# Optimization experiments

Hardware: AMD Instinct MI355X
Metric: run time of the kernel (lower is better)

The kernel has to match this reference:

```python
import jax, jax.numpy as jnp
import numpy as np

D_MODEL = 512
H = 8
D_K = D_MODEL // H
NEG = -1.0e9


def setup_inputs() -> dict:
    key = jax.random.key(0)
    ks = jax.random.split(key, 8)
    B, S = 2, 4096
    q = jax.random.normal(ks[0], (B, S, D_MODEL), dtype=jnp.float32)
    k = jax.random.normal(ks[1], (B, S, D_MODEL), dtype=jnp.float32)
    v = jax.random.normal(ks[2], (B, S, D_MODEL), dtype=jnp.float32)
    mask = jax.random.randint(ks[3], (B, 1, 1, S), 0, 2, dtype=jnp.int32)
    scale = 1.0 / np.sqrt(D_MODEL)
    w_q = jax.random.normal(ks[4], (D_MODEL, D_MODEL), dtype=jnp.float32) * scale
    w_k = jax.random.normal(ks[5], (D_MODEL, D_MODEL), dtype=jnp.float32) * scale
    w_v = jax.random.normal(ks[6], (D_MODEL, D_MODEL), dtype=jnp.float32) * scale
    w_o = jax.random.normal(ks[7], (D_MODEL, D_MODEL), dtype=jnp.float32) * scale
    return {"q": q, "k": k, "v": v, "mask": mask,
            "w_q": w_q, "w_k": w_k, "w_v": w_v, "w_o": w_o}


def reference(q, k, v, mask, w_q, w_k, w_v, w_o):
    B, S, _ = q.shape
    # nn.Linear(x) = x @ W.T; project and split heads -> [B, H, S, D_K]
    def split_heads(x, w):
        return (x @ w.T).reshape(B, -1, H, D_K).transpose(0, 2, 1, 3)
    query = split_heads(q, w_q)
    key_ = split_heads(k, w_k)
    value = split_heads(v, w_v)
    scores = jnp.einsum("bhqd,bhkd->bhqk", query, key_) / jnp.sqrt(
        jnp.asarray(D_K, dtype=q.dtype))
    scores = jnp.where(mask == 0, jnp.asarray(NEG, dtype=scores.dtype), scores)
    attn = jax.nn.softmax(scores, axis=-1)  # dropout p=0.0 (eval)
    x = jnp.einsum("bhqk,bhkd->bhqd", attn, value)
    x = x.transpose(0, 2, 1, 3).reshape(B, S, H * D_K)
    return x @ w_o.T
```

## Files before the change

### kernel.cpp

```cpp
#include <hip/hip_runtime.h>

typedef unsigned short u16;
typedef unsigned int u32;
typedef __attribute__((ext_vector_type(8))) short bf16x8;
typedef __attribute__((ext_vector_type(4))) float f32x4;
typedef __attribute__((ext_vector_type(2))) unsigned int u32x2;

__device__ __forceinline__ u16 f2bf(float f) {
  u32 u = __builtin_bit_cast(u32, f);
  u += 0x7fffu + ((u >> 16) & 1u);
  return (u16)(u >> 16);
}
__device__ __forceinline__ u32 pack2(float a, float b) {
  return (u32)f2bf(a) | ((u32)f2bf(b) << 16);
}
__device__ __forceinline__ u32 pack2_rhu(float a, float b) {
  u32 ua = __builtin_bit_cast(u32, a) + 0x8000u;
  u32 ub = __builtin_bit_cast(u32, b) + 0x8000u;
  return (ua >> 16) | (ub & 0xffff0000u);
}

__device__ __forceinline__ void gload_lds16(const u16* g, u16* l) {
  __builtin_amdgcn_global_load_lds(
      (const __attribute__((address_space(1))) void*)g,
      (__attribute__((address_space(3))) void*)l, 16, 0, 0);
}

__global__ __launch_bounds__(256) void wm_cvt(
    const float* __restrict__ wq, const float* __restrict__ wk,
    const float* __restrict__ wv, const float* __restrict__ wo,
    const int* __restrict__ mask, u16* __restrict__ Wb, u16* __restrict__ mbf) {
  int blk = blockIdx.x;
  if (blk < 1024) {
    int z = blk >> 8;
    const float* w = (z == 0) ? wq : (z == 1) ? wk : (z == 2) ? wv : wo;
    int i = (blk & 255) * 256 + threadIdx.x;
    f32x4 f = reinterpret_cast<const f32x4*>(w)[i];
    u32x2 o; o.x = pack2(f[0], f[1]); o.y = pack2(f[2], f[3]);
    reinterpret_cast<u32x2*>(Wb + (size_t)z * 262144)[i] = o;
  } else {
    int i = (blk - 1024) * 256 + threadIdx.x;
    mbf[i] = mask[i] ? (u16)0x3F80 : (u16)0;
  }
}

#define BM 128
#define BN 128
#define LDP 40

__global__ __launch_bounds__(256) void proj_gemm(
    const float* __restrict__ qf, const float* __restrict__ kf,
    const float* __restrict__ vf, const u16* __restrict__ Wb,
    const int* __restrict__ mask,
    u16* __restrict__ Qb, u16* __restrict__ Kb, u16* __restrict__ Vt)
{
  __shared__ u16 lds_a[BM * LDP];
  __shared__ u16 lds_b[BN * LDP];
  int z = blockIdx.z;
  const float* A = (z == 0) ? qf : (z == 1) ? kf : vf;
  const u16* W = Wb + (size_t)z * 262144;
  f32x4 acc[4][4] = {};
  int mtile = blockIdx.x * BM, ntile = blockIdx.y * BN;

  int tid = threadIdx.x;
  int lane = tid & 63;
  int w = tid >> 6;
  int wm = w >> 1, wn = w & 1;
  int ar = tid >> 2;
  int ac = (tid & 3) * 8;
  int lrow = lane & 15, lk = lane >> 4;

  for (int k0 = 0; k0 < 512; k0 += 32) {
    __syncthreads();
#pragma unroll
    for (int rr = 0; rr < BM; rr += 64) {
      const float* ap = A + (size_t)(mtile + ar + rr) * 512 + k0 + ac;
      f32x4 a0 = *reinterpret_cast<const f32x4*>(ap);
      f32x4 a1 = *reinterpret_cast<const f32x4*>(ap + 4);
      u32 q0 = pack2_rhu(a0[0], a0[1]), q1 = pack2_rhu(a0[2], a0[3]);
      u32 q2 = pack2_rhu(a1[0], a1[1]), q3 = pack2_rhu(a1[2], a1[3]);
      int4 va; va.x = (int)q0; va.y = (int)q1; va.z = (int)q2; va.w = (int)q3;
      *reinterpret_cast<int4*>(lds_a + (ar + rr) * LDP + ac) = va;
      int4 vb = *reinterpret_cast<const int4*>(W + (ntile + ar + rr) * 512 + k0 + ac);
      *reinterpret_cast<int4*>(lds_b + (ar + rr) * LDP + ac) = vb;
    }
    __syncthreads();
    bf16x8 af[4], bfr[4];
#pragma unroll
    for (int i = 0; i < 4; i++) {
      af[i]  = *reinterpret_cast<bf16x8*>(lds_a + (wm * 64 + i * 16 + lrow) * LDP + lk * 8);
      bfr[i] = *reinterpret_cast<bf16x8*>(lds_b + (wn * 64 + i * 16 + lrow) * LDP + lk * 8);
    }
#pragma unroll
    for (int i = 0; i < 4; i++)
#pragma unroll
      for (int j = 0; j < 4; j++)
        acc[i][j] = __builtin_amdgcn_mfma_f32_16x16x32_bf16(af[i], bfr[j], acc[i][j], 0, 0, 0);
  }

  u16* dst = (z == 0) ? Qb : (z == 1) ? Kb : Vt;
  float scl = (z == 0) ? 0.18033688011112042f : 1.0f;
#pragma unroll
  for (int i = 0; i < 4; i++)
#pragma unroll
    for (int j = 0; j < 4; j++)
#pragma unroll
      for (int r = 0; r < 4; r++) {
        int m = mtile + wm * 64 + i * 16 + lk * 4 + r;
        int n = ntile + wn * 64 + j * 16 + lrow;
        u16 bv = f2bf(acc[i][j][r] * scl);
        int b = m >> 12, s = m & 4095;
        int h = n >> 6, d = n & 63;
        if (z <= 1) dst[(((size_t)(b * 8 + h) * 4096 + s) * 64 + d)] = bv;
        else {
          if (mask[b * 4096 + s] == 0) bv = 0;
          dst[(((size_t)(b * 8 + h) * 64 + d) * 4096 + s)] = bv;
        }
      }
}

__global__ __launch_bounds__(256) void out_gemm(
    const u16* __restrict__ AO, const u16* __restrict__ Wo, float* __restrict__ out)
{
  __shared__ u16 lds_a[BM * LDP];
  __shared__ u16 lds_b[BN * LDP];
  f32x4 acc[4][4] = {};
  int mtile = blockIdx.x * BM, ntile = blockIdx.y * BN;

  int tid = threadIdx.x;
  int lane = tid & 63;
  int w = tid >> 6;
  int wm = w >> 1, wn = w & 1;
  int ar = tid >> 2;
  int ac = (tid & 3) * 8;
  int lrow = lane & 15, lk = lane >> 4;

  for (int k0 = 0; k0 < 512; k0 += 32) {
    __syncthreads();
#pragma unroll
    for (int rr = 0; rr < BM; rr += 64) {
      int4 va = *reinterpret_cast<const int4*>(AO + (size_t)(mtile + ar + rr) * 512 + k0 + ac);
      *reinterpret_cast<int4*>(lds_a + (ar + rr) * LDP + ac) = va;
      int4 vb = *reinterpret_cast<const int4*>(Wo + (size_t)(ntile + ar + rr) * 512 + k0 + ac);
      *reinterpret_cast<int4*>(lds_b + (ar + rr) * LDP + ac) = vb;
    }
    __syncthreads();
    bf16x8 af[4], bfr[4];
#pragma unroll
    for (int i = 0; i < 4; i++) {
      af[i]  = *reinterpret_cast<bf16x8*>(lds_a + (wm * 64 + i * 16 + lrow) * LDP + lk * 8);
      bfr[i] = *reinterpret_cast<bf16x8*>(lds_b + (wn * 64 + i * 16 + lrow) * LDP + lk * 8);
    }
#pragma unroll
    for (int i = 0; i < 4; i++)
#pragma unroll
      for (int j = 0; j < 4; j++)
        acc[i][j] = __builtin_amdgcn_mfma_f32_16x16x32_bf16(af[i], bfr[j], acc[i][j], 0, 0, 0);
  }

#pragma unroll
  for (int i = 0; i < 4; i++)
#pragma unroll
    for (int j = 0; j < 4; j++)
#pragma unroll
      for (int r = 0; r < 4; r++) {
        int m = mtile + wm * 64 + i * 16 + lk * 4 + r;
        int n = ntile + wn * 64 + j * 16 + lrow;
        out[(size_t)m * 512 + n] = acc[i][j][r];
      }
}

__global__ __launch_bounds__(512, 4) void attn_kernel(
    const u16* __restrict__ Qb, const u16* __restrict__ Kb,
    const u16* __restrict__ Vt, const u16* __restrict__ mbf,
    u16* __restrict__ AO)
{
  __shared__ u16 Kl[2][4096];
  __shared__ u16 Vl[2][4096];
  __shared__ u16 Pl[8][1024];
  int tid = threadIdx.x;
  int lane = tid & 63;
  int w = tid >> 6;
  int lrow = lane & 15, lk = lane >> 4;

  int lb = blockIdx.x;
  int bh = (lb & 7) * 2 + ((lb >> 3) & 1);
  int qt = lb >> 4;
  int b = bh >> 3, h = bh & 7;
  int q0 = qt * 128;

  const u16* Qp = Qb + ((size_t)bh * 4096 + q0 + w * 16 + lrow) * 64;
  bf16x8 bq0 = *(const bf16x8*)(Qp + lk * 8);
  bf16x8 bq1 = *(const bf16x8*)(Qp + 32 + lk * 8);

  const u16* Kbase = Kb + (size_t)bh * (4096 * 64);
  const u16* Vbase = Vt + (size_t)bh * (64 * 4096);
  const u16* mkb = mbf + b * 4096 + lk * 8;

  int trow = w * 8 + (lane >> 3);
  int tch  = (lane & 7) ^ (trow & 7);
  const u16* ksrc = Kbase + (size_t)trow * 64   + tch * 8;
  const u16* vsrc = Vbase + (size_t)trow * 4096 + tch * 8;
  u16* kdst = &Kl[0][0] + w * 512;
  u16* vdst = &Vl[0][0] + w * 512;

  int kc0 = (lk ^ (lrow & 7)) << 4;
  const char* kb0 = (const char*)&Kl[0][0] + lrow * 128 + kc0;
  const char* kb1 = (const char*)&Kl[0][0] + lrow * 128 + (kc0 ^ 64);
  const char* vb0 = (const char*)&Vl[0][0] + lrow * 128 + kc0;
  const char* vb1 = (const char*)&Vl[0][0] + lrow * 128 + (kc0 ^ 64);
  char* pw = (char*)(&Pl[w][0]);
  int pswz = (lrow & 7) << 4;
  char* pwa0 = pw + ((lrow * 128 +  0 + lk * 8) ^ pswz);
  char* pwa1 = pw + ((lrow * 128 + 32 + lk * 8) ^ pswz);
  char* pwa2 = pw + ((lrow * 128 + 64 + lk * 8) ^ pswz);
  char* pwa3 = pw + ((lrow * 128 + 96 + lk * 8) ^ pswz);
  const char* prd0 = pw + ((lrow * 128 +      lk * 16) ^ pswz);
  const char* prd1 = pw + ((lrow * 128 + 64 + lk * 16) ^ pswz);

  f32x4 o[4] = {};
  f32x4 ol = {};

  gload_lds16(ksrc, kdst);
  gload_lds16(vsrc, vdst);
  __syncthreads();

#define AITER(P, KT)                                                             \
  {                                                                              \
    if ((KT) + 64 < 4096) {                                                      \
      gload_lds16(ksrc + (size_t)((KT) + 64) * 64, kdst + ((P) ^ 1) * 4096);     \
      gload_lds16(vsrc + ((KT) + 64),              vdst + ((P) ^ 1) * 4096);     \
    }                                                                            \
    bf16x8 mb0 = *(const bf16x8*)(mkb + (KT));                                   \
    bf16x8 mb1 = *(const bf16x8*)(mkb + (KT) + 32);                              \
    f32x4 sc[4];                                                                 \
    __builtin_amdgcn_s_setprio(1);                                               \
    _Pragma("unroll")                                                            \
    for (int cb = 0; cb < 4; cb++) {                                             \
      bf16x8 ak0 = *(const bf16x8*)(kb0 + (P) * 8192 + cb * 2048);               \
      bf16x8 ak1 = *(const bf16x8*)(kb1 + (P) * 8192 + cb * 2048);               \
      f32x4 t = {};                                                              \
      t = __builtin_amdgcn_mfma_f32_16x16x32_bf16(ak0, bq0, t, 0, 0, 0);         \
      t = __builtin_amdgcn_mfma_f32_16x16x32_bf16(ak1, bq1, t, 0, 0, 0);         \
      sc[cb] = t;                                                                \
    }                                                                            \
    __builtin_amdgcn_s_setprio(0);                                               \
            \
    _Pragma("unroll")                                                            \
    for (int cb = 0; cb < 4; cb++) {                                             \
      float p0 = __builtin_amdgcn_exp2f(sc[cb][0]);                              \
      float p1 = __builtin_amdgcn_exp2f(sc[cb][1]);                              \
      float p2 = __builtin_amdgcn_exp2f(sc[cb][2]);                              \
      float p3 = __builtin_amdgcn_exp2f(sc[cb][3]);                              \
      u32x2 pk; pk.x = pack2_rhu(p0, p1); pk.y = pack2_rhu(p2, p3);              \
      *(u32x2*)(cb == 0 ? pwa0 : cb == 1 ? pwa1 : cb == 2 ? pwa2 : pwa3) = pk;   \
    }                                                                            \
    asm volatile("s_waitcnt lgkmcnt(0)" ::: "memory");                           \
    __builtin_amdgcn_sched_barrier(0);                                           \
    bf16x8 pb0 = *(const bf16x8*)prd0;                                           \
    bf16x8 pb1 = *(const bf16x8*)prd1;                                           \
    __builtin_amdgcn_s_setprio(1);                                               \
    _Pragma("unroll")                                                            \
    for (int nb = 0; nb < 4; nb++) {                                             \
      bf16x8 av0 = *(const bf16x8*)(vb0 + (P) * 8192 + nb * 2048);               \
      bf16x8 av1 = *(const bf16x8*)(vb1 + (P) * 8192 + nb * 2048);               \
      o[nb] = __builtin_amdgcn_mfma_f32_16x16x32_bf16(av0, pb0, o[nb], 0, 0, 0); \
      o[nb] = __builtin_amdgcn_mfma_f32_16x16x32_bf16(av1, pb1, o[nb], 0, 0, 0); \
    }                                                                            \
    ol = __builtin_amdgcn_mfma_f32_16x16x32_bf16(mb0, pb0, ol, 0, 0, 0);         \
    ol = __builtin_amdgcn_mfma_f32_16x16x32_bf16(mb1, pb1, ol, 0, 0, 0);         \
    __builtin_amdgcn_s_setprio(0);                                               \
    __syncthreads();                                                             \
  }

  for (int kt = 0; kt < 4096; kt += 128) {
    AITER(0, kt)
    AITER(1, kt + 64)
  }
#undef AITER

  float inv = 1.0f / ol[0];
  int srow = q0 + w * 16 + lrow;
#pragma unroll
  for (int nb = 0; nb < 4; nb++) {
    u32x2 pk;
    pk.x = pack2_rhu(o[nb][0] * inv, o[nb][1] * inv);
    pk.y = pack2_rhu(o[nb][2] * inv, o[nb][3] * inv);
    *(u32x2*)(AO + (size_t)(b * 4096 + srow) * 512 + h * 64 + nb * 16 + lk * 4) = pk;
  }
}

extern "C" void kernel_launch(void* const* d_in, const int* in_sizes, int n_in,
                              void* d_out, int out_size, void* d_ws, size_t ws_size,
                              hipStream_t stream) {
  const float* q  = (const float*)d_in[0];
  const float* k  = (const float*)d_in[1];
  const float* v  = (const float*)d_in[2];
  const int* mask = (const int*)d_in[3];
  const float* wq = (const float*)d_in[4];
  const float* wk = (const float*)d_in[5];
  const float* wv = (const float*)d_in[6];
  const float* wo = (const float*)d_in[7];
  float* out = (float*)d_out;

  u16* ws = (u16*)d_ws;
  u16* Wb = ws;
  u16* Qb = Wb + (size_t)4 * 262144;
  u16* Kb = Qb + 4194304;
  u16* Vt = Kb + 4194304;
  u16* AO = Vt + 4194304;
  u16* mbf = AO + 4194304;

  wm_cvt<<<1056, 256, 0, stream>>>(wq, wk, wv, wo, mask, Wb, mbf);
  proj_gemm<<<dim3(64, 4, 3), 256, 0, stream>>>(q, k, v, Wb, mask, Qb, Kb, Vt);
  attn_kernel<<<512, 512, 0, stream>>>(Qb, Kb, Vt, mbf, AO);
  out_gemm<<<dim3(64, 4), 256, 0, stream>>>(AO, Wb + 3 * 262144, out);
}
```

Before: 146.3 us.

## Process two 16-row query tiles per wave in attention, halving waves per block

The attention kernel now runs 4 waves per block instead of 8, and each wave handles 32 query rows as two 16-row sub-tiles. Each K and V fragment read from LDS feeds MFMAs for both sub-tiles, halving LDS reads per unit of work, and each thread issues twice as many global-to-LDS copies. The cost is higher register pressure per wave, fewer waves to hide latency, and a changed launch-bounds occupancy hint.

```diff
diff --git a/kernel.cpp b/kernel.cpp
--- a/kernel.cpp
+++ b/kernel.cpp
@@ -170,14 +170,14 @@
       }
 }
 
-__global__ __launch_bounds__(512, 4) void attn_kernel(
+__global__ __launch_bounds__(256, 2) void attn_kernel(
     const u16* __restrict__ Qb, const u16* __restrict__ Kb,
     const u16* __restrict__ Vt, const u16* __restrict__ mbf,
     u16* __restrict__ AO)
 {
   __shared__ u16 Kl[2][4096];
   __shared__ u16 Vl[2][4096];
-  __shared__ u16 Pl[8][1024];
+  __shared__ u16 Pl[4][2][1024];
   int tid = threadIdx.x;
   int lane = tid & 63;
   int w = tid >> 6;
@@ -189,88 +189,117 @@
   int b = bh >> 3, h = bh & 7;
   int q0 = qt * 128;
 
-  const u16* Qp = Qb + ((size_t)bh * 4096 + q0 + w * 16 + lrow) * 64;
-  bf16x8 bq0 = *(const bf16x8*)(Qp + lk * 8);
-  bf16x8 bq1 = *(const bf16x8*)(Qp + 32 + lk * 8);
+  const u16* Qp = Qb + ((size_t)bh * 4096 + q0 + w * 32 + lrow) * 64;
+  bf16x8 bqA0 = *(const bf16x8*)(Qp + lk * 8);
+  bf16x8 bqA1 = *(const bf16x8*)(Qp + 32 + lk * 8);
+  bf16x8 bqB0 = *(const bf16x8*)(Qp + 16 * 64 + lk * 8);
+  bf16x8 bqB1 = *(const bf16x8*)(Qp + 16 * 64 + 32 + lk * 8);
 
   const u16* Kbase = Kb + (size_t)bh * (4096 * 64);
   const u16* Vbase = Vt + (size_t)bh * (64 * 4096);
   const u16* mkb = mbf + b * 4096 + lk * 8;
 
-  int trow = w * 8 + (lane >> 3);
+  int trow = w * 16 + (lane >> 3);
   int tch  = (lane & 7) ^ (trow & 7);
-  const u16* ksrc = Kbase + (size_t)trow * 64   + tch * 8;
-  const u16* vsrc = Vbase + (size_t)trow * 4096 + tch * 8;
-  u16* kdst = &Kl[0][0] + w * 512;
-  u16* vdst = &Vl[0][0] + w * 512;
+  const u16* ksrc0 = Kbase + (size_t)trow * 64 + tch * 8;
+  const u16* ksrc1 = ksrc0 + 8 * 64;
+  const u16* vsrc0 = Vbase + (size_t)trow * 4096 + tch * 8;
+  const u16* vsrc1 = vsrc0 + 8 * 4096;
+  u16* kdst = &Kl[0][0] + w * 1024;
+  u16* vdst = &Vl[0][0] + w * 1024;
 
   int kc0 = (lk ^ (lrow & 7)) << 4;
   const char* kb0 = (const char*)&Kl[0][0] + lrow * 128 + kc0;
   const char* kb1 = (const char*)&Kl[0][0] + lrow * 128 + (kc0 ^ 64);
   const char* vb0 = (const char*)&Vl[0][0] + lrow * 128 + kc0;
   const char* vb1 = (const char*)&Vl[0][0] + lrow * 128 + (kc0 ^ 64);
-  char* pw = (char*)(&Pl[w][0]);
   int pswz = (lrow & 7) << 4;
-  char* pwa0 = pw + ((lrow * 128 +  0 + lk * 8) ^ pswz);
-  char* pwa1 = pw + ((lrow * 128 + 32 + lk * 8) ^ pswz);
-  char* pwa2 = pw + ((lrow * 128 + 64 + lk * 8) ^ pswz);
-  char* pwa3 = pw + ((lrow * 128 + 96 + lk * 8) ^ pswz);
-  const char* prd0 = pw + ((lrow * 128 +      lk * 16) ^ pswz);
-  const char* prd1 = pw + ((lrow * 128 + 64 + lk * 16) ^ pswz);
-
-  f32x4 o[4] = {};
-  f32x4 ol = {};
-
-  gload_lds16(ksrc, kdst);
-  gload_lds16(vsrc, vdst);
+  char* pwA = (char*)(&Pl[w][0][0]);
+  char* pwB = (char*)(&Pl[w][1][0]);
+  char* pwaA0 = pwA + ((lrow * 128 +  0 + lk * 8) ^ pswz);
+  char* pwaA1 = pwA + ((lrow * 128 + 32 + lk * 8) ^ pswz);
+  char* pwaA2 = pwA + ((lrow * 128 + 64 + lk * 8) ^ pswz);
+  char* pwaA3 = pwA + ((lrow * 128 + 96 + lk * 8) ^ pswz);
+  char* pwaB0 = pwB + ((lrow * 128 +  0 + lk * 8) ^ pswz);
+  char* pwaB1 = pwB + ((lrow * 128 + 32 + lk * 8) ^ pswz);
+  char* pwaB2 = pwB + ((lrow * 128 + 64 + lk * 8) ^ pswz);
+  char* pwaB3 = pwB + ((lrow * 128 + 96 + lk * 8) ^ pswz);
+  const char* prdA0 = pwA + ((lrow * 128 +      lk * 16) ^ pswz);
+  const char* prdA1 = pwA + ((lrow * 128 + 64 + lk * 16) ^ pswz);
+  const char* prdB0 = pwB + ((lrow * 128 +      lk * 16) ^ pswz);
+  const char* prdB1 = pwB + ((lrow * 128 + 64 + lk * 16) ^ pswz);
+
+  f32x4 oA[4] = {}, oB[4] = {};
+  f32x4 olA = {}, olB = {};
+
+  gload_lds16(ksrc0, kdst);
+  gload_lds16(ksrc1, kdst + 512);
+  gload_lds16(vsrc0, vdst);
+  gload_lds16(vsrc1, vdst + 512);
   __syncthreads();
 
-#define AITER(P, KT)                                                             \
-  {                                                                              \
-    if ((KT) + 64 < 4096) {                                                      \
-      gload_lds16(ksrc + (size_t)((KT) + 64) * 64, kdst + ((P) ^ 1) * 4096);     \
-      gload_lds16(vsrc + ((KT) + 64),              vdst + ((P) ^ 1) * 4096);     \
-    }                                                                            \
-    bf16x8 mb0 = *(const bf16x8*)(mkb + (KT));                                   \
-    bf16x8 mb1 = *(const bf16x8*)(mkb + (KT) + 32);                              \
-    f32x4 sc[4];                                                                 \
-    __builtin_amdgcn_s_setprio(1);                                               \
-    _Pragma("unroll")                                                            \
-    for (int cb = 0; cb < 4; cb++) {                                             \
-      bf16x8 ak0 = *(const bf16x8*)(kb0 + (P) * 8192 + cb * 2048);               \
-      bf16x8 ak1 = *(const bf16x8*)(kb1 + (P) * 8192 + cb * 2048);               \
-      f32x4 t = {};                                                              \
-      t = __builtin_amdgcn_mfma_f32_16x16x32_bf16(ak0, bq0, t, 0, 0, 0);         \
-      t = __builtin_amdgcn_mfma_f32_16x16x32_bf16(ak1, bq1, t, 0, 0, 0);         \
-      sc[cb] = t;                                                                \
-    }                                                                            \
-    __builtin_amdgcn_s_setprio(0);                                               \
-            \
-    _Pragma("unroll")                                                            \
-    for (int cb = 0; cb < 4; cb++) {                                             \
-      float p0 = __builtin_amdgcn_exp2f(sc[cb][0]);                              \
-      float p1 = __builtin_amdgcn_exp2f(sc[cb][1]);                              \
-      float p2 = __builtin_amdgcn_exp2f(sc[cb][2]);                              \
-      float p3 = __builtin_amdgcn_exp2f(sc[cb][3]);                              \
-      u32x2 pk; pk.x = pack2_rhu(p0, p1); pk.y = pack2_rhu(p2, p3);              \
-      *(u32x2*)(cb == 0 ? pwa0 : cb == 1 ? pwa1 : cb == 2 ? pwa2 : pwa3) = pk;   \
-    }                                                                            \
-    asm volatile("s_waitcnt lgkmcnt(0)" ::: "memory");                           \
-    __builtin_amdgcn_sched_barrier(0);                                           \
-    bf16x8 pb0 = *(const bf16x8*)prd0;                                           \
-    bf16x8 pb1 = *(const bf16x8*)prd1;                                           \
-    __builtin_amdgcn_s_setprio(1);                                               \
-    _Pragma("unroll")                                                            \
-    for (int nb = 0; nb < 4; nb++) {                                             \
-      bf16x8 av0 = *(const bf16x8*)(vb0 + (P) * 8192 + nb * 2048);               \
-      bf16x8 av1 = *(const bf16x8*)(vb1 + (P) * 8192 + nb * 2048);               \
-      o[nb] = __builtin_amdgcn_mfma_f32_16x16x32_bf16(av0, pb0, o[nb], 0, 0, 0); \
-      o[nb] = __builtin_amdgcn_mfma_f32_16x16x32_bf16(av1, pb1, o[nb], 0, 0, 0); \
-    }                                                                            \
-    ol = __builtin_amdgcn_mfma_f32_16x16x32_bf16(mb0, pb0, ol, 0, 0, 0);         \
-    ol = __builtin_amdgcn_mfma_f32_16x16x32_bf16(mb1, pb1, ol, 0, 0, 0);         \
-    __builtin_amdgcn_s_setprio(0);                                               \
-    __syncthreads();                                                             \
+#define AITER(P, KT)                                                               \
+  {                                                                                \
+    if ((KT) + 64 < 4096) {                                                        \
+      gload_lds16(ksrc0 + (size_t)((KT) + 64) * 64, kdst + ((P) ^ 1) * 4096);      \
+      gload_lds16(ksrc1 + (size_t)((KT) + 64) * 64, kdst + ((P) ^ 1) * 4096 + 512);\
+      gload_lds16(vsrc0 + ((KT) + 64),              vdst + ((P) ^ 1) * 4096);      \
+      gload_lds16(vsrc1 + ((KT) + 64),              vdst + ((P) ^ 1) * 4096 + 512);\
+    }                                                                              \
+    bf16x8 mb0 = *(const bf16x8*)(mkb + (KT));                                     \
+    bf16x8 mb1 = *(const bf16x8*)(mkb + (KT) + 32);                                \
+    f32x4 scA[4], scB[4];                                                          \
+    __builtin_amdgcn_s_setprio(1);                                                 \
+    _Pragma("unroll")                                                              \
+    for (int cb = 0; cb < 4; cb++) {                                               \
+      bf16x8 ak0 = *(const bf16x8*)(kb0 + (P) * 8192 + cb * 2048);                 \
+      bf16x8 ak1 = *(const bf16x8*)(kb1 + (P) * 8192 + cb * 2048);                 \
+      f32x4 tA = {}, tB = {};                                                      \
+      tA = __builtin_amdgcn_mfma_f32_16x16x32_bf16(ak0, bqA0, tA, 0, 0, 0);        \
+      tA = __builtin_amdgcn_mfma_f32_16x16x32_bf16(ak1, bqA1, tA, 0, 0, 0);        \
+      tB = __builtin_amdgcn_mfma_f32_16x16x32_bf16(ak0, bqB0, tB, 0, 0, 0);        \
+      tB = __builtin_amdgcn_mfma_f32_16x16x32_bf16(ak1, bqB1, tB, 0, 0, 0);        \
+      scA[cb] = tA; scB[cb] = tB;                                                  \
+    }                                                                              \
+    __builtin_amdgcn_s_setprio(0);                                                 \
+                       \
+    _Pragma("unroll")                                                              \
+    for (int cb = 0; cb < 4; cb++) {                                               \
+      float a0 = __builtin_amdgcn_exp2f(scA[cb][0]);                               \
+      float a1 = __builtin_amdgcn_exp2f(scA[cb][1]);                               \
+      float a2 = __builtin_amdgcn_exp2f(scA[cb][2]);                               \
+      float a3 = __builtin_amdgcn_exp2f(scA[cb][3]);                               \
+      u32x2 pkA; pkA.x = pack2_rhu(a0, a1); pkA.y = pack2_rhu(a2, a3);             \
+      *(u32x2*)(cb == 0 ? pwaA0 : cb == 1 ? pwaA1 : cb == 2 ? pwaA2 : pwaA3) = pkA;\
+      float b0 = __builtin_amdgcn_exp2f(scB[cb][0]);                               \
+      float b1 = __builtin_amdgcn_exp2f(scB[cb][1]);                               \
+      float b2 = __builtin_amdgcn_exp2f(scB[cb][2]);                               \
+      float b3 = __builtin_amdgcn_exp2f(scB[cb][3]);                               \
+      u32x2 pkB; pkB.x = pack2_rhu(b0, b1); pkB.y = pack2_rhu(b2, b3);             \
+      *(u32x2*)(cb == 0 ? pwaB0 : cb == 1 ? pwaB1 : cb == 2 ? pwaB2 : pwaB3) = pkB;\
+    }                                                                              \
+    asm volatile("s_waitcnt lgkmcnt(0)" ::: "memory");                             \
+    __builtin_amdgcn_sched_barrier(0);                                             \
+    bf16x8 pbA0 = *(const bf16x8*)prdA0;                                           \
+    bf16x8 pbA1 = *(const bf16x8*)prdA1;                                           \
+    bf16x8 pbB0 = *(const bf16x8*)prdB0;                                           \
+    bf16x8 pbB1 = *(const bf16x8*)prdB1;                                           \
+    __builtin_amdgcn_s_setprio(1);                                                 \
+    _Pragma("unroll")                                                              \
+    for (int nb = 0; nb < 4; nb++) {                                               \
+      bf16x8 av0 = *(const bf16x8*)(vb0 + (P) * 8192 + nb * 2048);                 \
+      bf16x8 av1 = *(const bf16x8*)(vb1 + (P) * 8192 + nb * 2048);                 \
+      oA[nb] = __builtin_amdgcn_mfma_f32_16x16x32_bf16(av0, pbA0, oA[nb], 0, 0, 0);\
+      oA[nb] = __builtin_amdgcn_mfma_f32_16x16x32_bf16(av1, pbA1, oA[nb], 0, 0, 0);\
+      oB[nb] = __builtin_amdgcn_mfma_f32_16x16x32_bf16(av0, pbB0, oB[nb], 0, 0, 0);\
+      oB[nb] = __builtin_amdgcn_mfma_f32_16x16x32_bf16(av1, pbB1, oB[nb], 0, 0, 0);\
+    }                                                                              \
+    olA = __builtin_amdgcn_mfma_f32_16x16x32_bf16(mb0, pbA0, olA, 0, 0, 0);        \
+    olA = __builtin_amdgcn_mfma_f32_16x16x32_bf16(mb1, pbA1, olA, 0, 0, 0);        \
+    olB = __builtin_amdgcn_mfma_f32_16x16x32_bf16(mb0, pbB0, olB, 0, 0, 0);        \
+    olB = __builtin_amdgcn_mfma_f32_16x16x32_bf16(mb1, pbB1, olB, 0, 0, 0);        \
+    __builtin_amdgcn_s_setprio(0);                                                 \
+    __syncthreads();                                                               \
   }
 
   for (int kt = 0; kt < 4096; kt += 128) {
@@ -279,14 +308,19 @@
   }
 #undef AITER
 
-  float inv = 1.0f / ol[0];
-  int srow = q0 + w * 16 + lrow;
+  float invA = 1.0f / olA[0];
+  float invB = 1.0f / olB[0];
+  int srowA = q0 + w * 32 + lrow;
 #pragma unroll
   for (int nb = 0; nb < 4; nb++) {
-    u32x2 pk;
-    pk.x = pack2_rhu(o[nb][0] * inv, o[nb][1] * inv);
-    pk.y = pack2_rhu(o[nb][2] * inv, o[nb][3] * inv);
-    *(u32x2*)(AO + (size_t)(b * 4096 + srow) * 512 + h * 64 + nb * 16 + lk * 4) = pk;
+    u32x2 pkA;
+    pkA.x = pack2_rhu(oA[nb][0] * invA, oA[nb][1] * invA);
+    pkA.y = pack2_rhu(oA[nb][2] * invA, oA[nb][3] * invA);
+    *(u32x2*)(AO + (size_t)(b * 4096 + srowA) * 512 + h * 64 + nb * 16 + lk * 4) = pkA;
+    u32x2 pkB;
+    pkB.x = pack2_rhu(oB[nb][0] * invB, oB[nb][1] * invB);
+    pkB.y = pack2_rhu(oB[nb][2] * invB, oB[nb][3] * invB);
+    *(u32x2*)(AO + (size_t)(b * 4096 + srowA + 16) * 512 + h * 64 + nb * 16 + lk * 4) = pkB;
   }
 }
 
@@ -313,6 +347,6 @@
 
   wm_cvt<<<1056, 256, 0, stream>>>(wq, wk, wv, wo, mask, Wb, mbf);
   proj_gemm<<<dim3(64, 4, 3), 256, 0, stream>>>(q, k, v, Wb, mask, Qb, Kb, Vt);
-  attn_kernel<<<512, 512, 0, stream>>>(Qb, Kb, Vt, mbf, AO);
+  attn_kernel<<<512, 256, 0, stream>>>(Qb, Kb, Vt, mbf, AO);
   out_gemm<<<dim3(64, 4), 256, 0, stream>>>(AO, Wb + 3 * 262144, out);
 }
```

Measured after the change: 147.8 us. About the same (+1.0%).

## Switch attention to 32x32 MFMA tiles and split KV across blocks

Applied to the files above, without the earlier changes.

Rewrites the attention kernel to use 32x32x16 bf16 MFMAs with 32 query rows per wave (256 per block). It also splits the key range into two halves across blocks, with partial outputs and row sums accumulated via float atomics into a zeroed fp32 buffer, then normalized and packed to bf16 by a new combine kernel. The larger MFMA tiles aim to reduce LDS operand traffic per flop and improve matrix-core efficiency. In exchange it adds a memset, about 4M atomic adds, an extra kernel launch and larger fp32 intermediate traffic.

```diff
diff --git a/kernel.cpp b/kernel.cpp
--- a/kernel.cpp
+++ b/kernel.cpp
@@ -4,6 +4,7 @@
 typedef unsigned int u32;
 typedef __attribute__((ext_vector_type(8))) short bf16x8;
 typedef __attribute__((ext_vector_type(4))) float f32x4;
+typedef __attribute__((ext_vector_type(16))) float f32x16;
 typedef __attribute__((ext_vector_type(2))) unsigned int u32x2;
 
 __device__ __forceinline__ u16 f2bf(float f) {
@@ -170,32 +171,35 @@
       }
 }
 
-__global__ __launch_bounds__(512, 4) void attn_kernel(
+__global__ __launch_bounds__(512, 4) void attn32(
     const u16* __restrict__ Qb, const u16* __restrict__ Kb,
     const u16* __restrict__ Vt, const u16* __restrict__ mbf,
-    u16* __restrict__ AO)
+    float* __restrict__ obuf, float* __restrict__ lbuf)
 {
   __shared__ u16 Kl[2][4096];
   __shared__ u16 Vl[2][4096];
-  __shared__ u16 Pl[8][1024];
+  __shared__ u16 Pl[8][2048];
   int tid = threadIdx.x;
   int lane = tid & 63;
   int w = tid >> 6;
-  int lrow = lane & 15, lk = lane >> 4;
+  int lq = lane & 31, hi = lane >> 5;
 
   int lb = blockIdx.x;
   int bh = (lb & 7) * 2 + ((lb >> 3) & 1);
-  int qt = lb >> 4;
-  int b = bh >> 3, h = bh & 7;
-  int q0 = qt * 128;
-
-  const u16* Qp = Qb + ((size_t)bh * 4096 + q0 + w * 16 + lrow) * 64;
-  bf16x8 bq0 = *(const bf16x8*)(Qp + lk * 8);
-  bf16x8 bq1 = *(const bf16x8*)(Qp + 32 + lk * 8);
+  int qt = (lb >> 4) & 15;
+  int half = lb >> 8;
+  int b = bh >> 3;
+  int qw = qt * 256 + w * 32;
+  int kt0 = half * 2048, ktend = kt0 + 2048;
+
+  const u16* Qp = Qb + ((size_t)bh * 4096 + qw + lq) * 64 + hi * 8;
+  bf16x8 bq[4];
+#pragma unroll
+  for (int dd = 0; dd < 4; dd++) bq[dd] = *(const bf16x8*)(Qp + 16 * dd);
 
   const u16* Kbase = Kb + (size_t)bh * (4096 * 64);
   const u16* Vbase = Vt + (size_t)bh * (64 * 4096);
-  const u16* mkb = mbf + b * 4096 + lk * 8;
+  const u16* mkb = mbf + b * 4096 + hi * 8;
 
   int trow = w * 8 + (lane >> 3);
   int tch  = (lane & 7) ^ (trow & 7);
@@ -204,90 +208,111 @@
   u16* kdst = &Kl[0][0] + w * 512;
   u16* vdst = &Vl[0][0] + w * 512;
 
-  int kc0 = (lk ^ (lrow & 7)) << 4;
-  const char* kb0 = (const char*)&Kl[0][0] + lrow * 128 + kc0;
-  const char* kb1 = (const char*)&Kl[0][0] + lrow * 128 + (kc0 ^ 64);
-  const char* vb0 = (const char*)&Vl[0][0] + lrow * 128 + kc0;
-  const char* vb1 = (const char*)&Vl[0][0] + lrow * 128 + (kc0 ^ 64);
-  char* pw = (char*)(&Pl[w][0]);
-  int pswz = (lrow & 7) << 4;
-  char* pwa0 = pw + ((lrow * 128 +  0 + lk * 8) ^ pswz);
-  char* pwa1 = pw + ((lrow * 128 + 32 + lk * 8) ^ pswz);
-  char* pwa2 = pw + ((lrow * 128 + 64 + lk * 8) ^ pswz);
-  char* pwa3 = pw + ((lrow * 128 + 96 + lk * 8) ^ pswz);
-  const char* prd0 = pw + ((lrow * 128 +      lk * 16) ^ pswz);
-  const char* prd1 = pw + ((lrow * 128 + 64 + lk * 16) ^ pswz);
-
-  f32x4 o[4] = {};
-  f32x4 ol = {};
-
-  gload_lds16(ksrc, kdst);
-  gload_lds16(vsrc, vdst);
+  int xoff[4];
+#pragma unroll
+  for (int i = 0; i < 4; i++) xoff[i] = (((hi ^ (lq & 7)) << 4) ^ (i << 5));
+  const char* klp = (const char*)&Kl[0][0] + lq * 128;
+  const char* vlp = (const char*)&Vl[0][0] + lq * 128;
+  char* plw = (char*)(&Pl[w][0]) + lq * 128;
+  int pwoff[4];
+#pragma unroll
+  for (int w2 = 0; w2 < 4; w2++) pwoff[w2] = (((w2 ^ (lq & 7)) << 4) + hi * 8);
+
+  f32x16 o0 = {}, o1 = {};
+  f32x16 ol = {};
+
+  gload_lds16(ksrc + (size_t)kt0 * 64, kdst);
+  gload_lds16(vsrc + kt0,              vdst);
   __syncthreads();
 
-#define AITER(P, KT)                                                             \
-  {                                                                              \
-    if ((KT) + 64 < 4096) {                                                      \
-      gload_lds16(ksrc + (size_t)((KT) + 64) * 64, kdst + ((P) ^ 1) * 4096);     \
-      gload_lds16(vsrc + ((KT) + 64),              vdst + ((P) ^ 1) * 4096);     \
-    }                                                                            \
-    bf16x8 mb0 = *(const bf16x8*)(mkb + (KT));                                   \
-    bf16x8 mb1 = *(const bf16x8*)(mkb + (KT) + 32);                              \
-    f32x4 sc[4];                                                                 \
-    __builtin_amdgcn_s_setprio(1);                                               \
-    _Pragma("unroll")                                                            \
-    for (int cb = 0; cb < 4; cb++) {                                             \
-      bf16x8 ak0 = *(const bf16x8*)(kb0 + (P) * 8192 + cb * 2048);               \
-      bf16x8 ak1 = *(const bf16x8*)(kb1 + (P) * 8192 + cb * 2048);               \
-      f32x4 t = {};                                                              \
-      t = __builtin_amdgcn_mfma_f32_16x16x32_bf16(ak0, bq0, t, 0, 0, 0);         \
-      t = __builtin_amdgcn_mfma_f32_16x16x32_bf16(ak1, bq1, t, 0, 0, 0);         \
-      sc[cb] = t;                                                                \
-    }                                                                            \
-    __builtin_amdgcn_s_setprio(0);                                               \
-            \
-    _Pragma("unroll")                                                            \
-    for (int cb = 0; cb < 4; cb++) {                                             \
-      float p0 = __builtin_amdgcn_exp2f(sc[cb][0]);                              \
-      float p1 = __builtin_amdgcn_exp2f(sc[cb][1]);                              \
-      float p2 = __builtin_amdgcn_exp2f(sc[cb][2]);                              \
-      float p3 = __builtin_amdgcn_exp2f(sc[cb][3]);                              \
-      u32x2 pk; pk.x = pack2_rhu(p0, p1); pk.y = pack2_rhu(p2, p3);              \
-      *(u32x2*)(cb == 0 ? pwa0 : cb == 1 ? pwa1 : cb == 2 ? pwa2 : pwa3) = pk;   \
-    }                                                                            \
-    asm volatile("s_waitcnt lgkmcnt(0)" ::: "memory");                           \
-    __builtin_amdgcn_sched_barrier(0);                                           \
-    bf16x8 pb0 = *(const bf16x8*)prd0;                                           \
-    bf16x8 pb1 = *(const bf16x8*)prd1;                                           \
-    __builtin_amdgcn_s_setprio(1);                                               \
-    _Pragma("unroll")                                                            \
-    for (int nb = 0; nb < 4; nb++) {                                             \
-      bf16x8 av0 = *(const bf16x8*)(vb0 + (P) * 8192 + nb * 2048);               \
-      bf16x8 av1 = *(const bf16x8*)(vb1 + (P) * 8192 + nb * 2048);               \
-      o[nb] = __builtin_amdgcn_mfma_f32_16x16x32_bf16(av0, pb0, o[nb], 0, 0, 0); \
-      o[nb] = __builtin_amdgcn_mfma_f32_16x16x32_bf16(av1, pb1, o[nb], 0, 0, 0); \
-    }                                                                            \
-    ol = __builtin_amdgcn_mfma_f32_16x16x32_bf16(mb0, pb0, ol, 0, 0, 0);         \
-    ol = __builtin_amdgcn_mfma_f32_16x16x32_bf16(mb1, pb1, ol, 0, 0, 0);         \
-    __builtin_amdgcn_s_setprio(0);                                               \
-    __syncthreads();                                                             \
-  }
-
-  for (int kt = 0; kt < 4096; kt += 128) {
+#define AITER(P, KT)                                                               \
+  {                                                                                \
+    if ((KT) + 64 < ktend) {                                                       \
+      gload_lds16(ksrc + (size_t)((KT) + 64) * 64, kdst + ((P) ^ 1) * 4096);       \
+      gload_lds16(vsrc + ((KT) + 64),              vdst + ((P) ^ 1) * 4096);       \
+    }                                                                              \
+    bf16x8 mb[4];                                                                  \
+    _Pragma("unroll")                                                              \
+    for (int kk = 0; kk < 4; kk++) mb[kk] = *(const bf16x8*)(mkb + (KT) + 16 * kk);\
+    f32x16 s0 = {}, s1 = {};                                                       \
+    __builtin_amdgcn_s_setprio(1);                                                 \
+    _Pragma("unroll")                                                              \
+    for (int dd = 0; dd < 4; dd++) {                                               \
+      bf16x8 ak0 = *(const bf16x8*)(klp + (P) * 8192 +        xoff[dd]);           \
+      bf16x8 ak1 = *(const bf16x8*)(klp + (P) * 8192 + 4096 + xoff[dd]);           \
+      s0 = __builtin_amdgcn_mfma_f32_32x32x16_bf16(ak0, bq[dd], s0, 0, 0, 0);      \
+      s1 = __builtin_amdgcn_mfma_f32_32x32x16_bf16(ak1, bq[dd], s1, 0, 0, 0);      \
+    }                                                                              \
+    __builtin_amdgcn_s_setprio(0);                                                 \
+     \
+    _Pragma("unroll")                                                              \
+    for (int w2 = 0; w2 < 4; w2++) {                                               \
+      u32x2 pk;                                                                    \
+      pk.x = pack2_rhu(__builtin_amdgcn_exp2f(s0[4 * w2 + 0]),                     \
+                       __builtin_amdgcn_exp2f(s0[4 * w2 + 1]));                    \
+      pk.y = pack2_rhu(__builtin_amdgcn_exp2f(s0[4 * w2 + 2]),                     \
+                       __builtin_amdgcn_exp2f(s0[4 * w2 + 3]));                    \
+      *(u32x2*)(plw + pwoff[w2]) = pk;                                             \
+      u32x2 pk1;                                                                   \
+      pk1.x = pack2_rhu(__builtin_amdgcn_exp2f(s1[4 * w2 + 0]),                    \
+                        __builtin_amdgcn_exp2f(s1[4 * w2 + 1]));                   \
+      pk1.y = pack2_rhu(__builtin_amdgcn_exp2f(s1[4 * w2 + 2]),                    \
+                        __builtin_amdgcn_exp2f(s1[4 * w2 + 3]));                   \
+      *(u32x2*)(plw + (pwoff[w2] ^ 64)) = pk1;                                     \
+    }                                                                              \
+    asm volatile("s_waitcnt lgkmcnt(0)" ::: "memory");                             \
+    __builtin_amdgcn_sched_barrier(0);                                             \
+    bf16x8 pb[4];                                                                  \
+    _Pragma("unroll")                                                              \
+    for (int kk = 0; kk < 4; kk++) pb[kk] = *(const bf16x8*)(plw + xoff[kk]);      \
+    __builtin_amdgcn_s_setprio(1);                                                 \
+    _Pragma("unroll")                                                              \
+    for (int kk = 0; kk < 4; kk++) {                                               \
+      bf16x8 av0 = *(const bf16x8*)(vlp + (P) * 8192 +        xoff[kk]);           \
+      bf16x8 av1 = *(const bf16x8*)(vlp + (P) * 8192 + 4096 + xoff[kk]);           \
+      o0 = __builtin_amdgcn_mfma_f32_32x32x16_bf16(av0, pb[kk], o0, 0, 0, 0);      \
+      o1 = __builtin_amdgcn_mfma_f32_32x32x16_bf16(av1, pb[kk], o1, 0, 0, 0);      \
+      ol = __builtin_amdgcn_mfma_f32_32x32x16_bf16(mb[kk], pb[kk], ol, 0, 0, 0);   \
+    }                                                                              \
+    __builtin_amdgcn_s_setprio(0);                                                 \
+    __syncthreads();                                                               \
+  }
+
+  for (int kt = kt0; kt < ktend; kt += 128) {
     AITER(0, kt)
     AITER(1, kt + 64)
   }
 #undef AITER
 
-  float inv = 1.0f / ol[0];
-  int srow = q0 + w * 16 + lrow;
-#pragma unroll
-  for (int nb = 0; nb < 4; nb++) {
-    u32x2 pk;
-    pk.x = pack2_rhu(o[nb][0] * inv, o[nb][1] * inv);
-    pk.y = pack2_rhu(o[nb][2] * inv, o[nb][3] * inv);
-    *(u32x2*)(AO + (size_t)(b * 4096 + srow) * 512 + h * 64 + nb * 16 + lk * 4) = pk;
-  }
+  float* ob = obuf + ((size_t)bh * 4096 + qw + lq) * 64;
+#pragma unroll
+  for (int r = 0; r < 16; r++) {
+    int d = (r & 3) + 8 * (r >> 2) + 4 * hi;
+    atomicAdd(ob + d, o0[r]);
+    atomicAdd(ob + d + 32, o1[r]);
+  }
+  if (hi == 0) atomicAdd(lbuf + bh * 4096 + qw + lq, ol[0]);
+}
+
+__global__ __launch_bounds__(256) void combine(
+    const float* __restrict__ obuf, const float* __restrict__ lbuf,
+    u16* __restrict__ AO)
+{
+  int gid = blockIdx.x * 256 + threadIdx.x;
+  int qi = gid >> 3;
+  int dc = gid & 7;
+  const float* op = obuf + (size_t)qi * 64 + dc * 8;
+  f32x4 a = *(const f32x4*)op;
+  f32x4 c = *(const f32x4*)(op + 4);
+  float inv = 1.0f / lbuf[qi];
+  int bh = qi >> 12, s = qi & 4095;
+  int4 pk;
+  pk.x = (int)pack2_rhu(a[0] * inv, a[1] * inv);
+  pk.y = (int)pack2_rhu(a[2] * inv, a[3] * inv);
+  pk.z = (int)pack2_rhu(c[0] * inv, c[1] * inv);
+  pk.w = (int)pack2_rhu(c[2] * inv, c[3] * inv);
+  u16* dst = AO + ((size_t)((bh >> 3) * 4096 + s)) * 512 + (bh & 7) * 64 + dc * 8;
+  *(int4*)dst = pk;
 }
 
 extern "C" void kernel_launch(void* const* d_in, const int* in_sizes, int n_in,
@@ -310,9 +335,13 @@
   u16* Vt = Kb + 4194304;
   u16* AO = Vt + 4194304;
   u16* mbf = AO + 4194304;
+  float* obuf = (float*)(mbf + 8192);
+  float* lbuf = obuf + (size_t)4194304;
 
   wm_cvt<<<1056, 256, 0, stream>>>(wq, wk, wv, wo, mask, Wb, mbf);
   proj_gemm<<<dim3(64, 4, 3), 256, 0, stream>>>(q, k, v, Wb, mask, Qb, Kb, Vt);
-  attn_kernel<<<512, 512, 0, stream>>>(Qb, Kb, Vt, mbf, AO);
+  hipMemsetAsync(obuf, 0, (size_t)(4194304 + 65536) * 4, stream);
+  attn32<<<512, 512, 0, stream>>>(Qb, Kb, Vt, mbf, obuf, lbuf);
+  combine<<<2048, 256, 0, stream>>>(obuf, lbuf, AO);
   out_gemm<<<dim3(64, 4), 256, 0, stream>>>(AO, Wb + 3 * 262144, out);
 }
```

After: 436.6 us. 2.98x slower.

## Software-pipeline attention: overlap QK of next tile with PV of previous

Applied to the files above, without the earlier changes.

The attention loop is restructured so that each iteration computes QK scores for the current key tile while running the P·V and mask-sum MFMAs for the previous tile. K/V LDS staging moves from double to triple buffering, with a prologue that computes the first tile's probabilities and an epilogue that drains the last P·V. The goal is to hide the exp/pack/LDS round-trip latency behind matrix work and to need only one barrier per tile. The cost is more LDS per block (64KB instead of 48KB), which may cut resident blocks per CU, plus more live registers.

```diff
diff --git a/kernel.cpp b/kernel.cpp
--- a/kernel.cpp
+++ b/kernel.cpp
@@ -175,8 +175,8 @@
     const u16* __restrict__ Vt, const u16* __restrict__ mbf,
     u16* __restrict__ AO)
 {
-  __shared__ u16 Kl[2][4096];
-  __shared__ u16 Vl[2][4096];
+  __shared__ u16 Kl[3][4096];
+  __shared__ u16 Vl[3][4096];
   __shared__ u16 Pl[8][1024];
   int tid = threadIdx.x;
   int lane = tid & 63;
@@ -220,32 +220,72 @@
 
   f32x4 o[4] = {};
   f32x4 ol = {};
+  bf16x8 pb0, pb1;
 
   gload_lds16(ksrc, kdst);
   gload_lds16(vsrc, vdst);
   __syncthreads();
-
-#define AITER(P, KT)                                                             \
+  gload_lds16(ksrc + (size_t)64 * 64, kdst + 4096);
+  gload_lds16(vsrc + 64,              vdst + 4096);
+  {
+    f32x4 sc[4];
+    __builtin_amdgcn_s_setprio(1);
+#pragma unroll
+    for (int cb = 0; cb < 4; cb++) {
+      bf16x8 ak0 = *(const bf16x8*)(kb0 + cb * 2048);
+      bf16x8 ak1 = *(const bf16x8*)(kb1 + cb * 2048);
+      f32x4 t = {};
+      t = __builtin_amdgcn_mfma_f32_16x16x32_bf16(ak0, bq0, t, 0, 0, 0);
+      t = __builtin_amdgcn_mfma_f32_16x16x32_bf16(ak1, bq1, t, 0, 0, 0);
+      sc[cb] = t;
+    }
+    __builtin_amdgcn_s_setprio(0);
+#pragma unroll
+    for (int cb = 0; cb < 4; cb++) {
+      float p0 = __builtin_amdgcn_exp2f(sc[cb][0]);
+      float p1 = __builtin_amdgcn_exp2f(sc[cb][1]);
+      float p2 = __builtin_amdgcn_exp2f(sc[cb][2]);
+      float p3 = __builtin_amdgcn_exp2f(sc[cb][3]);
+      u32x2 pk; pk.x = pack2_rhu(p0, p1); pk.y = pack2_rhu(p2, p3);
+      *(u32x2*)(cb == 0 ? pwa0 : cb == 1 ? pwa1 : cb == 2 ? pwa2 : pwa3) = pk;
+    }
+    asm volatile("s_waitcnt lgkmcnt(0)" ::: "memory");
+    __builtin_amdgcn_sched_barrier(0);
+    pb0 = *(const bf16x8*)prd0;
+    pb1 = *(const bf16x8*)prd1;
+  }
+
+#define AITER(CUR, PRV, NXT, KT)                                                 \
   {                                                                              \
+    __syncthreads();   \
     if ((KT) + 64 < 4096) {                                                      \
-      gload_lds16(ksrc + (size_t)((KT) + 64) * 64, kdst + ((P) ^ 1) * 4096);     \
-      gload_lds16(vsrc + ((KT) + 64),              vdst + ((P) ^ 1) * 4096);     \
+      gload_lds16(ksrc + (size_t)((KT) + 64) * 64, kdst + (NXT) * 4096);         \
+      gload_lds16(vsrc + ((KT) + 64),              vdst + (NXT) * 4096);         \
     }                                                                            \
-    bf16x8 mb0 = *(const bf16x8*)(mkb + (KT));                                   \
-    bf16x8 mb1 = *(const bf16x8*)(mkb + (KT) + 32);                              \
     f32x4 sc[4];                                                                 \
     __builtin_amdgcn_s_setprio(1);                                               \
     _Pragma("unroll")                                                            \
     for (int cb = 0; cb < 4; cb++) {                                             \
-      bf16x8 ak0 = *(const bf16x8*)(kb0 + (P) * 8192 + cb * 2048);               \
-      bf16x8 ak1 = *(const bf16x8*)(kb1 + (P) * 8192 + cb * 2048);               \
+      bf16x8 ak0 = *(const bf16x8*)(kb0 + (CUR) * 8192 + cb * 2048);             \
+      bf16x8 ak1 = *(const bf16x8*)(kb1 + (CUR) * 8192 + cb * 2048);             \
       f32x4 t = {};                                                              \
       t = __builtin_amdgcn_mfma_f32_16x16x32_bf16(ak0, bq0, t, 0, 0, 0);         \
       t = __builtin_amdgcn_mfma_f32_16x16x32_bf16(ak1, bq1, t, 0, 0, 0);         \
       sc[cb] = t;                                                                \
     }                                                                            \
+        \
+    bf16x8 mb0 = *(const bf16x8*)(mkb + (KT) - 64);                              \
+    bf16x8 mb1 = *(const bf16x8*)(mkb + (KT) - 32);                              \
+    _Pragma("unroll")                                                            \
+    for (int nb = 0; nb < 4; nb++) {                                             \
+      bf16x8 av0 = *(const bf16x8*)(vb0 + (PRV) * 8192 + nb * 2048);             \
+      bf16x8 av1 = *(const bf16x8*)(vb1 + (PRV) * 8192 + nb * 2048);             \
+      o[nb] = __builtin_amdgcn_mfma_f32_16x16x32_bf16(av0, pb0, o[nb], 0, 0, 0); \
+      o[nb] = __builtin_amdgcn_mfma_f32_16x16x32_bf16(av1, pb1, o[nb], 0, 0, 0); \
+    }                                                                            \
+    ol = __builtin_amdgcn_mfma_f32_16x16x32_bf16(mb0, pb0, ol, 0, 0, 0);         \
+    ol = __builtin_amdgcn_mfma_f32_16x16x32_bf16(mb1, pb1, ol, 0, 0, 0);         \
     __builtin_amdgcn_s_setprio(0);                                               \
-            \
     _Pragma("unroll")                                                            \
     for (int cb = 0; cb < 4; cb++) {                                             \
       float p0 = __builtin_amdgcn_exp2f(sc[cb][0]);                              \
@@ -257,27 +297,32 @@
     }                                                                            \
     asm volatile("s_waitcnt lgkmcnt(0)" ::: "memory");                           \
     __builtin_amdgcn_sched_barrier(0);                                           \
-    bf16x8 pb0 = *(const bf16x8*)prd0;                                           \
-    bf16x8 pb1 = *(const bf16x8*)prd1;                                           \
-    __builtin_amdgcn_s_setprio(1);                                               \
-    _Pragma("unroll")                                                            \
-    for (int nb = 0; nb < 4; nb++) {                                             \
-      bf16x8 av0 = *(const bf16x8*)(vb0 + (P) * 8192 + nb * 2048);               \
-      bf16x8 av1 = *(const bf16x8*)(vb1 + (P) * 8192 + nb * 2048);               \
-      o[nb] = __builtin_amdgcn_mfma_f32_16x16x32_bf16(av0, pb0, o[nb], 0, 0, 0); \
-      o[nb] = __builtin_amdgcn_mfma_f32_16x16x32_bf16(av1, pb1, o[nb], 0, 0, 0); \
-    }                                                                            \
-    ol = __builtin_amdgcn_mfma_f32_16x16x32_bf16(mb0, pb0, ol, 0, 0, 0);         \
-    ol = __builtin_amdgcn_mfma_f32_16x16x32_bf16(mb1, pb1, ol, 0, 0, 0);         \
-    __builtin_amdgcn_s_setprio(0);                                               \
-    __syncthreads();                                                             \
-  }
-
-  for (int kt = 0; kt < 4096; kt += 128) {
-    AITER(0, kt)
-    AITER(1, kt + 64)
+    pb0 = *(const bf16x8*)prd0;                                                  \
+    pb1 = *(const bf16x8*)prd1;                                                  \
+  }
+
+  for (int kt = 64; kt < 4096; kt += 192) {
+    AITER(1, 0, 2, kt)
+    AITER(2, 1, 0, kt + 64)
+    AITER(0, 2, 1, kt + 128)
   }
 #undef AITER
+
+  {
+    bf16x8 mb0 = *(const bf16x8*)(mkb + 4032);
+    bf16x8 mb1 = *(const bf16x8*)(mkb + 4064);
+    __builtin_amdgcn_s_setprio(1);
+#pragma unroll
+    for (int nb = 0; nb < 4; nb++) {
+      bf16x8 av0 = *(const bf16x8*)(vb0 + nb * 2048);
+      bf16x8 av1 = *(const bf16x8*)(vb1 + nb * 2048);
+      o[nb] = __builtin_amdgcn_mfma_f32_16x16x32_bf16(av0, pb0, o[nb], 0, 0, 0);
+      o[nb] = __builtin_amdgcn_mfma_f32_16x16x32_bf16(av1, pb1, o[nb], 0, 0, 0);
+    }
+    ol = __builtin_amdgcn_mfma_f32_16x16x32_bf16(mb0, pb0, ol, 0, 0, 0);
+    ol = __builtin_amdgcn_mfma_f32_16x16x32_bf16(mb1, pb1, ol, 0, 0, 0);
+    __builtin_amdgcn_s_setprio(0);
+  }
 
   float inv = 1.0f / ol[0];
   int srow = q0 + w * 16 + lrow;
```

Measured after the change: 145.1 us. No clear change (-0.9%).
